# Performance work log

Measured on AMD Instinct MI355X. Metric: run time of the kernel, lower is better.

Reference implementation:

```python
import jax, jax.numpy as jnp
import numpy as np


def positional_encoding(n_tokens, d_model, dtype=jnp.float32):
    # standard sinusoidal PE: pe[pos, 2i] = sin(pos / 10000^(2i/d)), pe[pos, 2i+1] = cos(...)
    pos = jnp.arange(n_tokens, dtype=dtype)[:, None]            # [n, 1]
    i = jnp.arange(0, d_model, 2, dtype=dtype)[None, :]         # [1, d/2]
    angle = pos / jnp.power(jnp.asarray(10000.0, dtype), i / d_model)
    pe = jnp.zeros((n_tokens, d_model), dtype)
    pe = pe.at[:, 0::2].set(jnp.sin(angle))
    pe = pe.at[:, 1::2].set(jnp.cos(angle))
    return pe


def layer_norm(x, gamma, beta, eps=1e-5):
    mu = jnp.mean(x, axis=-1, keepdims=True)
    var = jnp.var(x, axis=-1, keepdims=True)
    return (x - mu) * jax.lax.rsqrt(var + eps) * gamma + beta


def setup_inputs() -> dict:
    key = jax.random.key(0)
    ks = jax.random.split(key, 4)
    b, n, d = 4, 1024, 1024
    dh = 1024  # dim_hidden_linear
    s = 1.0 / np.sqrt(d)
    return {
        "token_embedding": jax.random.normal(ks[0], (b, n, d), jnp.float32),
        "ln_gamma": jnp.ones((d,), jnp.float32),
        "ln_beta": jnp.zeros((d,), jnp.float32),
        "Wq": jax.random.normal(ks[1], (d, dh), jnp.float32) * s,
        "bq": jnp.zeros((dh,), jnp.float32),
        "Wk": jax.random.normal(ks[2], (d, dh), jnp.float32) * s,
        "bk": jnp.zeros((dh,), jnp.float32),
        "Wv": jax.random.normal(ks[3], (d, dh), jnp.float32) * s,
        "bv": jnp.zeros((dh,), jnp.float32),
        "num_heads": 16,
    }


def reference(token_embedding, ln_gamma, ln_beta, Wq, bq, Wk, bk, Wv, bv, num_heads):
    b, n, d = token_embedding.shape
    pe = positional_encoding(n, d)                      # [n, d]
    x = token_embedding + pe[None, :, :]                # broadcast over batch
    x = layer_norm(x, ln_gamma, ln_beta)
    q = x @ Wq + bq                                     # [b, n, dh]
    k = x @ Wk + bk
    v = x @ Wv + bv
    dh = q.shape[-1]
    hd = dh // num_heads                                # per-head dim
    q = q.reshape(b, n, num_heads, hd)
    k = k.reshape(b, n, num_heads, hd)
    v = v.reshape(b, n, num_heads, hd)
    scale = 1.0 / jnp.sqrt(jnp.asarray(hd, q.dtype))
    scores = jnp.einsum("bqhd,bkhd->bhqk", q, k) * scale  # [b, h, n, n]
    attn = jax.nn.softmax(scores, axis=-1)
    out = jnp.einsum("bhqk,bkhd->bqhd", attn, v)          # [b, n, h, hd]
    return out.reshape(b, n, dh)
```

## Files before the change

### kernel.cpp

```cpp
#include <hip/hip_runtime.h>
#include <hip/hip_bf16.h>
#include <math.h>

typedef __attribute__((ext_vector_type(8))) short bf16x8;
typedef __attribute__((ext_vector_type(4))) short bf16x4;
typedef __attribute__((ext_vector_type(4))) float f32x4;

static __device__ __forceinline__ void gld16(const void* g, void* l) {
    __builtin_amdgcn_global_load_lds(
        (const __attribute__((address_space(1))) unsigned int*)g,
        (__attribute__((address_space(3))) unsigned int*)l, 16, 0, 0);
}

static __device__ __forceinline__ short f2bf_s(float f) {
    __hip_bfloat16 h = __float2bfloat16(f);
    short s;
    __builtin_memcpy(&s, &h, 2);
    return s;
}

__global__ __launch_bounds__(256) void peln_wt_kernel(
    const float* __restrict__ emb,
    const float* __restrict__ gamma,
    const float* __restrict__ beta,
    const float* __restrict__ Wq,
    const float* __restrict__ Wk,
    const float* __restrict__ Wv,
    __hip_bfloat16* __restrict__ x,
    __hip_bfloat16* __restrict__ Wt)
{
    const int tid = threadIdx.x;
    if (blockIdx.x < 4096) {
        const int row = blockIdx.x;
        const int t   = row & 1023;
        float4 e = ((const float4*)(emb + (size_t)row * 1024))[tid];
        float v[4] = {e.x, e.y, e.z, e.w};
        float s = 0.f, ss = 0.f;
        #pragma unroll
        for (int kk = 0; kk < 4; ++kk) {
            int c = tid * 4 + kk;
            float ang = (float)t * exp2f(-13.287712379549449f * (float)(c >> 1) * (1.0f / 512.0f));
            float pe  = (c & 1) ? __cosf(ang) : __sinf(ang);
            v[kk] += pe;
            s  += v[kk];
            ss += v[kk] * v[kk];
        }
        #pragma unroll
        for (int off = 1; off < 64; off <<= 1) {
            s  += __shfl_xor(s, off);
            ss += __shfl_xor(ss, off);
        }
        __shared__ float red_s[4], red_ss[4];
        int wave = tid >> 6, lane = tid & 63;
        if (lane == 0) { red_s[wave] = s; red_ss[wave] = ss; }
        __syncthreads();
        float S  = red_s[0] + red_s[1] + red_s[2] + red_s[3];
        float SS = red_ss[0] + red_ss[1] + red_ss[2] + red_ss[3];
        float mu   = S * (1.0f / 1024.0f);
        float var  = SS * (1.0f / 1024.0f) - mu * mu;
        float rstd = rsqrtf(var + 1e-5f);
        #pragma unroll
        for (int kk = 0; kk < 4; ++kk) {
            int c = tid * 4 + kk;
            float y = (v[kk] - mu) * rstd * gamma[c] + beta[c];
            x[(size_t)row * 1024 + c] = __float2bfloat16(y);
        }
    } else {
        __shared__ __hip_bfloat16 tile[32][33];
        int wid = blockIdx.x - 4096;
        int zz  = wid >> 10;
        int rem = wid & 1023;
        int bx = rem & 31, by = rem >> 5;
        int tx = tid & 31, ty = tid >> 5;
        const float* src = (zz == 0) ? Wq : (zz == 1) ? Wk : Wv;
        __hip_bfloat16* dst = Wt + (size_t)zz * 1024 * 1024;
        int x0 = bx * 32, y0 = by * 32;
        #pragma unroll
        for (int kk = 0; kk < 4; ++kk)
            tile[ty + 8 * kk][tx] =
                __float2bfloat16(src[(size_t)(y0 + ty + 8 * kk) * 1024 + x0 + tx]);
        __syncthreads();
        #pragma unroll
        for (int kk = 0; kk < 4; ++kk)
            dst[(size_t)(x0 + ty + 8 * kk) * 1024 + y0 + tx] = tile[tx][ty + 8 * kk];
    }
}

__global__ __launch_bounds__(256) void qkv_gemm(
    const __hip_bfloat16* __restrict__ X,
    const __hip_bfloat16* __restrict__ Wt,
    const float* __restrict__ bq,
    const float* __restrict__ bk,
    const float* __restrict__ bv,
    __hip_bfloat16* __restrict__ qkv,
    __hip_bfloat16* __restrict__ vt)
{
    union SMem {
        struct { __hip_bfloat16 A[128 * 64]; __hip_bfloat16 B[128 * 64]; } s;
        __hip_bfloat16 C[128 * 132];
    };
    __shared__ __align__(16) SMem sm;

    const int id   = blockIdx.x;
    const int xcd  = id & 7;
    const int rest = id >> 3;
    const int j    = rest % 3;
    const int mblk = rest / 3;
    const int m0   = mblk * 128;
    const int n0   = (xcd * 3 + j) * 128;
    const int t    = n0 >> 10;
    const int nn0  = n0 & 1023;
    const __hip_bfloat16* W = Wt + (size_t)t * 1024 * 1024;

    const int tid  = threadIdx.x;
    const int wave = tid >> 6, lane = tid & 63;
    const int wm = wave & 1, wn = wave >> 1;
    const int lm = lane & 15, quad = lane >> 4;

    const int srow = lane >> 3;
    const int skc  = ((lane & 7) ^ srow) * 8;
    const int rbase = wave * 32;
    const __hip_bfloat16* gA = X + (size_t)(m0 + rbase + srow) * 1024 + skc;
    const __hip_bfloat16* gB = W + (size_t)(nn0 + rbase + srow) * 1024 + skc;
    __hip_bfloat16* lA = sm.s.A + rbase * 64;
    __hip_bfloat16* lB = sm.s.B + rbase * 64;

    f32x4 acc[4][4];
    #pragma unroll
    for (int i = 0; i < 4; ++i)
        #pragma unroll
        for (int jj = 0; jj < 4; ++jj)
            acc[i][jj] = (f32x4){0.f, 0.f, 0.f, 0.f};

    for (int k0 = 0; k0 < 1024; k0 += 64) {
        #pragma unroll
        for (int n = 0; n < 4; ++n) {
            gld16(gA + (size_t)n * 8 * 1024 + k0, lA + n * 8 * 64);
            gld16(gB + (size_t)n * 8 * 1024 + k0, lB + n * 8 * 64);
        }
        __syncthreads();

        bf16x8 a[2][4], b[2][4];
        #pragma unroll
        for (int ks = 0; ks < 2; ++ks) {
            #pragma unroll
            for (int i = 0; i < 4; ++i) {
                int row = wm * 64 + i * 16 + lm;
                a[ks][i] = *(const bf16x8*)(sm.s.A + (size_t)row * 64
                                            + (((ks * 4 + quad) ^ (lm & 7)) * 8));
            }
            #pragma unroll
            for (int jj = 0; jj < 4; ++jj) {
                int row = wn * 64 + jj * 16 + lm;
                b[ks][jj] = *(const bf16x8*)(sm.s.B + (size_t)row * 64
                                             + (((ks * 4 + quad) ^ (lm & 7)) * 8));
            }
        }
        __syncthreads();

        #pragma unroll
        for (int ks = 0; ks < 2; ++ks)
            #pragma unroll
            for (int i = 0; i < 4; ++i)
                #pragma unroll
                for (int jj = 0; jj < 4; ++jj)
                    acc[i][jj] = __builtin_amdgcn_mfma_f32_16x16x32_bf16(a[ks][i], b[ks][jj], acc[i][jj], 0, 0, 0);
    }

    const float* bias = (t == 0) ? bq : (t == 1) ? bk : bv;
    if (t < 2) {
        #pragma unroll
        for (int jj = 0; jj < 4; ++jj) {
            int col = wn * 64 + jj * 16 + lm;
            float bb = bias[nn0 + col];
            #pragma unroll
            for (int i = 0; i < 4; ++i)
                #pragma unroll
                for (int r = 0; r < 4; ++r) {
                    int row = wm * 64 + i * 16 + quad * 4 + r;
                    sm.C[(size_t)row * 132 + col] = __float2bfloat16(acc[i][jj][r] + bb);
                }
        }
        __syncthreads();
        __hip_bfloat16* out = qkv + (size_t)t * 4096 * 1024;
        #pragma unroll
        for (int c = 0; c < 8; ++c) {
            int g = tid + 256 * c;
            int row = g >> 4;
            int colc = (g & 15) * 8;
            bf16x8 vch = *(const bf16x8*)&sm.C[(size_t)row * 132 + colc];
            *(bf16x8*)(out + (size_t)(m0 + row) * 1024 + nn0 + colc) = vch;
        }
    } else {
        #pragma unroll
        for (int jj = 0; jj < 4; ++jj) {
            int col = wn * 64 + jj * 16 + lm;
            float bb = bias[nn0 + col];
            #pragma unroll
            for (int i = 0; i < 4; ++i)
                #pragma unroll
                for (int r = 0; r < 4; ++r) {
                    int row = wm * 64 + i * 16 + quad * 4 + r;
                    sm.C[(size_t)col * 132 + row] = __float2bfloat16(acc[i][jj][r] + bb);
                }
        }
        __syncthreads();
        const int bbase = (m0 >> 10) * 16 + (nn0 >> 6);
        const int mloc  = m0 & 1023;
        #pragma unroll
        for (int c = 0; c < 8; ++c) {
            int g = tid + 256 * c;
            int col = g >> 4;
            int rch = (g & 15) * 8;
            bf16x8 vch = *(const bf16x8*)&sm.C[(size_t)col * 132 + rch];
            int bh = bbase + (col >> 6);
            int d  = col & 63;
            *(bf16x8*)(vt + ((size_t)bh * 64 + d) * 1024 + mloc + rch) = vch;
        }
    }
}

__global__ __launch_bounds__(256, 2) void attn_kernel(
    const __hip_bfloat16* __restrict__ q,
    const __hip_bfloat16* __restrict__ k,
    const __hip_bfloat16* __restrict__ vt,
    float* __restrict__ out)
{
    __shared__ __align__(16) __hip_bfloat16 Kbuf[128 * 64];
    __shared__ __align__(16) __hip_bfloat16 Vbuf[2][64 * 64];
    __shared__ short ldsPT[4][32][72];
    const int id   = blockIdx.x;
    const int bh   = (id & 7) * 8 + ((id >> 3) & 7);
    const int qblk = id >> 6;
    const int b = bh >> 4, h = bh & 15;
    const int wave = threadIdx.x >> 6, lane = threadIdx.x & 63;
    const int lm = lane & 15, quad = lane >> 4;
    const int qbase = qblk * 128 + wave * 32;
    const float CEXP = 0.18033688011112042f;

    bf16x8 bqf[2][2];
    #pragma unroll
    for (int i = 0; i < 2; ++i)
        #pragma unroll
        for (int ks = 0; ks < 2; ++ks)
            bqf[i][ks] = *(const bf16x8*)(q + (size_t)(b * 1024 + qbase + 16 * i + lm) * 1024
                                            + h * 64 + ks * 32 + quad * 8);

    const __hip_bfloat16* kg = k + (size_t)(b * 1024) * 1024 + h * 64;
    const __hip_bfloat16* vg = vt + (size_t)bh * 64 * 1024;
    const int srow = lane >> 3;
    const int skc  = ((lane & 7) ^ srow) * 8;

    f32x4 OT[4][2];
    float li[2] = {0.f, 0.f};
    #pragma unroll
    for (int nt = 0; nt < 4; ++nt)
        #pragma unroll
        for (int i = 0; i < 2; ++i)
            OT[nt][i] = (f32x4){0.f, 0.f, 0.f, 0.f};

    for (int kt = 0; kt < 1024; kt += 128) {
        #pragma unroll
        for (int n = 0; n < 4; ++n) {
            int r0 = wave * 32 + n * 8;
            gld16(kg + (size_t)(kt + r0 + srow) * 1024 + skc, Kbuf + r0 * 64);
        }
        {
            int half = wave >> 1;
            #pragma unroll
            for (int n = 0; n < 4; ++n) {
                int d0 = (wave & 1) * 32 + n * 8;
                gld16(vg + (size_t)(d0 + srow) * 1024 + kt + half * 64 + skc,
                      Vbuf[half] + d0 * 64);
            }
        }
        __syncthreads();

        #pragma unroll
        for (int sr = 0; sr < 2; ++sr) {
            bf16x8 ak[4][2], av[4][2];
            #pragma unroll
            for (int jt = 0; jt < 4; ++jt)
                #pragma unroll
                for (int ks = 0; ks < 2; ++ks)
                    ak[jt][ks] = *(const bf16x8*)(Kbuf + (size_t)(sr * 64 + 16 * jt + lm) * 64
                                                  + (((ks * 4 + quad) ^ (lm & 7)) * 8));
            #pragma unroll
            for (int nt = 0; nt < 4; ++nt)
                #pragma unroll
                for (int ks = 0; ks < 2; ++ks)
                    av[nt][ks] = *(const bf16x8*)(Vbuf[sr] + (size_t)(16 * nt + lm) * 64
                                                  + (((ks * 4 + quad) ^ (lm & 7)) * 8));
            if (sr == 1) __syncthreads();

            f32x4 ST[2][4];
            #pragma unroll
            for (int i = 0; i < 2; ++i)
                #pragma unroll
                for (int jt = 0; jt < 4; ++jt)
                    ST[i][jt] = (f32x4){0.f, 0.f, 0.f, 0.f};
            #pragma unroll
            for (int ks = 0; ks < 2; ++ks)
                #pragma unroll
                for (int i = 0; i < 2; ++i)
                    #pragma unroll
                    for (int jt = 0; jt < 4; ++jt)
                        ST[i][jt] = __builtin_amdgcn_mfma_f32_16x16x32_bf16(ak[jt][ks], bqf[i][ks], ST[i][jt], 0, 0, 0);

            #pragma unroll
            for (int i = 0; i < 2; ++i)
                #pragma unroll
                for (int jt = 0; jt < 4; ++jt) {
                    bf16x4 pk;
                    #pragma unroll
                    for (int r = 0; r < 4; ++r) {
                        float p = __builtin_amdgcn_exp2f(ST[i][jt][r] * CEXP);
                        li[i] += p;
                        pk[r] = f2bf_s(p);
                    }
                    *(bf16x4*)&ldsPT[wave][16 * i + lm][16 * jt + quad * 4] = pk;
                }

            bf16x8 bp[2][2];
            #pragma unroll
            for (int i = 0; i < 2; ++i)
                #pragma unroll
                for (int ks = 0; ks < 2; ++ks)
                    bp[i][ks] = *(const bf16x8*)&ldsPT[wave][16 * i + lm][ks * 32 + quad * 8];
            #pragma unroll
            for (int ks = 0; ks < 2; ++ks)
                #pragma unroll
                for (int nt = 0; nt < 4; ++nt)
                    #pragma unroll
                    for (int i = 0; i < 2; ++i)
                        OT[nt][i] = __builtin_amdgcn_mfma_f32_16x16x32_bf16(av[nt][ks], bp[i][ks], OT[nt][i], 0, 0, 0);
        }
    }

    #pragma unroll
    for (int i = 0; i < 2; ++i) {
        li[i] += __shfl_xor(li[i], 16);
        li[i] += __shfl_xor(li[i], 32);
    }

    #pragma unroll
    for (int i = 0; i < 2; ++i) {
        float inv = 1.0f / li[i];
        int qrow = qbase + 16 * i + lm;
        #pragma unroll
        for (int nt = 0; nt < 4; ++nt) {
            float4 o4 = {OT[nt][i][0] * inv, OT[nt][i][1] * inv,
                         OT[nt][i][2] * inv, OT[nt][i][3] * inv};
            *(float4*)(out + (size_t)(b * 1024 + qrow) * 1024 + h * 64 + 16 * nt + quad * 4) = o4;
        }
    }
}

extern "C" void kernel_launch(void* const* d_in, const int* in_sizes, int n_in,
                              void* d_out, int out_size, void* d_ws, size_t ws_size,
                              hipStream_t stream)
{
    const float* emb   = (const float*)d_in[0];
    const float* gamma = (const float*)d_in[1];
    const float* beta  = (const float*)d_in[2];
    const float* Wq    = (const float*)d_in[3];
    const float* bq    = (const float*)d_in[4];
    const float* Wk    = (const float*)d_in[5];
    const float* bk    = (const float*)d_in[6];
    const float* Wv    = (const float*)d_in[7];
    const float* bv    = (const float*)d_in[8];
    float* out = (float*)d_out;

    __hip_bfloat16* ws  = (__hip_bfloat16*)d_ws;
    __hip_bfloat16* x   = ws;
    __hip_bfloat16* Wt  = x   + (size_t)4096 * 1024;
    __hip_bfloat16* qkv = Wt  + (size_t)3 * 1024 * 1024;
    __hip_bfloat16* vt  = qkv + (size_t)2 * 4096 * 1024;

    peln_wt_kernel<<<4096 + 3072, 256, 0, stream>>>(emb, gamma, beta, Wq, Wk, Wv, x, Wt);
    qkv_gemm<<<768, 256, 0, stream>>>(x, Wt, bq, bk, bv, qkv, vt);
    attn_kernel<<<512, 256, 0, stream>>>(qkv, qkv + (size_t)4096 * 1024, vt, out);
}
```

Measured before the change: 156.0 us.

## Shrink attention key tile to 64 and raise occupancy to four blocks

After: 158.5 us. About the same (+1.6%).

```diff
diff --git a/kernel.cpp b/kernel.cpp
--- a/kernel.cpp
+++ b/kernel.cpp
@@ -220,15 +220,15 @@
     }
 }
 
-__global__ __launch_bounds__(256, 2) void attn_kernel(
+__global__ __launch_bounds__(256, 4) void attn_kernel(
     const __hip_bfloat16* __restrict__ q,
     const __hip_bfloat16* __restrict__ k,
     const __hip_bfloat16* __restrict__ vt,
     float* __restrict__ out)
 {
-    __shared__ __align__(16) __hip_bfloat16 Kbuf[128 * 64];
-    __shared__ __align__(16) __hip_bfloat16 Vbuf[2][64 * 64];
-    __shared__ short ldsPT[4][32][72];
+    __shared__ __align__(16) __hip_bfloat16 Kbuf[64 * 64];
+    __shared__ __align__(16) __hip_bfloat16 Vbuf[64 * 64];
+    __shared__ short ldsPT[4][32][66];
     const int id   = blockIdx.x;
     const int bh   = (id & 7) * 8 + ((id >> 3) & 7);
     const int qblk = id >> 6;
@@ -259,82 +259,67 @@
         for (int i = 0; i < 2; ++i)
             OT[nt][i] = (f32x4){0.f, 0.f, 0.f, 0.f};
 
-    for (int kt = 0; kt < 1024; kt += 128) {
-        #pragma unroll
-        for (int n = 0; n < 4; ++n) {
-            int r0 = wave * 32 + n * 8;
+    for (int kt = 0; kt < 1024; kt += 64) {
+        {
+            int r0 = wave * 16;
             gld16(kg + (size_t)(kt + r0 + srow) * 1024 + skc, Kbuf + r0 * 64);
-        }
-        {
-            int half = wave >> 1;
-            #pragma unroll
-            for (int n = 0; n < 4; ++n) {
-                int d0 = (wave & 1) * 32 + n * 8;
-                gld16(vg + (size_t)(d0 + srow) * 1024 + kt + half * 64 + skc,
-                      Vbuf[half] + d0 * 64);
+            gld16(kg + (size_t)(kt + r0 + 8 + srow) * 1024 + skc, Kbuf + (r0 + 8) * 64);
+            gld16(vg + (size_t)(r0 + srow) * 1024 + kt + skc, Vbuf + r0 * 64);
+            gld16(vg + (size_t)(r0 + 8 + srow) * 1024 + kt + skc, Vbuf + (r0 + 8) * 64);
+        }
+        __syncthreads();
+
+        f32x4 ST[2][4];
+        #pragma unroll
+        for (int i = 0; i < 2; ++i)
+            #pragma unroll
+            for (int jt = 0; jt < 4; ++jt)
+                ST[i][jt] = (f32x4){0.f, 0.f, 0.f, 0.f};
+        #pragma unroll
+        for (int ks = 0; ks < 2; ++ks) {
+            bf16x8 ak[4];
+            #pragma unroll
+            for (int jt = 0; jt < 4; ++jt)
+                ak[jt] = *(const bf16x8*)(Kbuf + (size_t)(16 * jt + lm) * 64
+                                          + (((ks * 4 + quad) ^ (lm & 7)) * 8));
+            #pragma unroll
+            for (int i = 0; i < 2; ++i)
+                #pragma unroll
+                for (int jt = 0; jt < 4; ++jt)
+                    ST[i][jt] = __builtin_amdgcn_mfma_f32_16x16x32_bf16(ak[jt], bqf[i][ks], ST[i][jt], 0, 0, 0);
+        }
+
+        #pragma unroll
+        for (int i = 0; i < 2; ++i)
+            #pragma unroll
+            for (int jt = 0; jt < 4; ++jt) {
+                bf16x4 pk;
+                #pragma unroll
+                for (int r = 0; r < 4; ++r) {
+                    float p = __builtin_amdgcn_exp2f(ST[i][jt][r] * CEXP);
+                    li[i] += p;
+                    pk[r] = f2bf_s(p);
+                }
+                *(bf16x4*)&ldsPT[wave][16 * i + lm][16 * jt + quad * 4] = pk;
             }
-        }
-        __syncthreads();
-
-        #pragma unroll
-        for (int sr = 0; sr < 2; ++sr) {
-            bf16x8 ak[4][2], av[4][2];
-            #pragma unroll
-            for (int jt = 0; jt < 4; ++jt)
-                #pragma unroll
-                for (int ks = 0; ks < 2; ++ks)
-                    ak[jt][ks] = *(const bf16x8*)(Kbuf + (size_t)(sr * 64 + 16 * jt + lm) * 64
-                                                  + (((ks * 4 + quad) ^ (lm & 7)) * 8));
+
+        #pragma unroll
+        for (int ks = 0; ks < 2; ++ks) {
+            bf16x8 bp[2], av[4];
+            #pragma unroll
+            for (int i = 0; i < 2; ++i)
+                bp[i] = *(const bf16x8*)&ldsPT[wave][16 * i + lm][ks * 32 + quad * 8];
             #pragma unroll
             for (int nt = 0; nt < 4; ++nt)
-                #pragma unroll
-                for (int ks = 0; ks < 2; ++ks)
-                    av[nt][ks] = *(const bf16x8*)(Vbuf[sr] + (size_t)(16 * nt + lm) * 64
-                                                  + (((ks * 4 + quad) ^ (lm & 7)) * 8));
-            if (sr == 1) __syncthreads();
-
-            f32x4 ST[2][4];
-            #pragma unroll
-            for (int i = 0; i < 2; ++i)
-                #pragma unroll
-                for (int jt = 0; jt < 4; ++jt)
-                    ST[i][jt] = (f32x4){0.f, 0.f, 0.f, 0.f};
-            #pragma unroll
-            for (int ks = 0; ks < 2; ++ks)
+                av[nt] = *(const bf16x8*)(Vbuf + (size_t)(16 * nt + lm) * 64
+                                          + (((ks * 4 + quad) ^ (lm & 7)) * 8));
+            #pragma unroll
+            for (int nt = 0; nt < 4; ++nt)
                 #pragma unroll
                 for (int i = 0; i < 2; ++i)
-                    #pragma unroll
-                    for (int jt = 0; jt < 4; ++jt)
-                        ST[i][jt] = __builtin_amdgcn_mfma_f32_16x16x32_bf16(ak[jt][ks], bqf[i][ks], ST[i][jt], 0, 0, 0);
-
-            #pragma unroll
-            for (int i = 0; i < 2; ++i)
-                #pragma unroll
-                for (int jt = 0; jt < 4; ++jt) {
-                    bf16x4 pk;
-                    #pragma unroll
-                    for (int r = 0; r < 4; ++r) {
-                        float p = __builtin_amdgcn_exp2f(ST[i][jt][r] * CEXP);
-                        li[i] += p;
-                        pk[r] = f2bf_s(p);
-                    }
-                    *(bf16x4*)&ldsPT[wave][16 * i + lm][16 * jt + quad * 4] = pk;
-                }
-
-            bf16x8 bp[2][2];
-            #pragma unroll
-            for (int i = 0; i < 2; ++i)
-                #pragma unroll
-                for (int ks = 0; ks < 2; ++ks)
-                    bp[i][ks] = *(const bf16x8*)&ldsPT[wave][16 * i + lm][ks * 32 + quad * 8];
-            #pragma unroll
-            for (int ks = 0; ks < 2; ++ks)
-                #pragma unroll
-                for (int nt = 0; nt < 4; ++nt)
-                    #pragma unroll
-                    for (int i = 0; i < 2; ++i)
-                        OT[nt][i] = __builtin_amdgcn_mfma_f32_16x16x32_bf16(av[nt][ks], bp[i][ks], OT[nt][i], 0, 0, 0);
-        }
+                    OT[nt][i] = __builtin_amdgcn_mfma_f32_16x16x32_bf16(av[nt], bp[i], OT[nt][i], 0, 0, 0);
+        }
+        __syncthreads();
     }
 
     #pragma unroll
```
